# Kernel tuning notes

Measured on AMD Instinct MI355X. Metric: run time of the kernel, lower is better.

The kernel has to match this reference:

```python
import jax, jax.numpy as jnp
import numpy as np

B, S = 2048, 512
VOCAB, MAXPOS = 50000, 512
DE = 50          # each embedding dim; concat -> 100
DIN, H, OUT = 100, 512, 2


def setup_inputs() -> dict:
    key = jax.random.key(0)
    ks = jax.random.split(key, 12)
    inp = {
        "emb_table": jax.random.normal(ks[0], (VOCAB, DE), jnp.float32) * 0.02,
        "pos_table": jax.random.normal(ks[1], (MAXPOS, DE), jnp.float32) * 0.02,
        "W1": jax.random.normal(ks[2], (DIN, H), jnp.float32) / np.sqrt(DIN),
        "b1": jnp.zeros((H,), jnp.float32),
        "W2": jax.random.normal(ks[3], (H, H), jnp.float32) / np.sqrt(H),
        "b2": jnp.zeros((H,), jnp.float32),
        "W3": jax.random.normal(ks[4], (H, H), jnp.float32) / np.sqrt(H),
        "b3": jnp.zeros((H,), jnp.float32),
        "Wf": jax.random.normal(ks[5], (H, OUT), jnp.float32) / np.sqrt(H),
        "bf": jnp.zeros((OUT,), jnp.float32),
        "seq": jax.random.randint(ks[6], (B, S), 0, VOCAB),
        "seq_length": jax.random.randint(ks[7], (B,), 1, S + 1),  # >=1 to avoid div-by-zero, as in real data
        "pos": jnp.tile(jnp.arange(S, dtype=jnp.int64 if jax.config.jax_enable_x64 else jnp.int32)[None, :], (B, 1)),
    }
    return inp


def reference(emb_table, pos_table, W1, b1, W2, b2, W3, b3, Wf, bf,
              seq, seq_length, pos):
    # Embedding lookups + concat on feature dim -> [B, S, 100]
    x = jnp.concatenate([emb_table[seq], pos_table[pos]], axis=2)
    # Masked mean over the first seq_length[i] tokens (replaces the Python double loop)
    mask = (jnp.arange(S)[None, :] < seq_length[:, None]).astype(x.dtype)  # [B, S]
    pooled = jnp.einsum("bsd,bs->bd", x, mask) / seq_length[:, None].astype(x.dtype)  # [B, 100]
    # MLP stack (Dropout p=0.5 is identity in eval mode)
    h = jax.nn.relu(pooled @ W1 + b1)
    h = jax.nn.relu(h @ W2 + b2)
    h = jax.nn.relu(h @ W3 + b3)
    return h @ Wf + bf  # [B, OUT]
```

## Files before the change

### kernel.cpp

```cpp
#include <hip/hip_runtime.h>

typedef __attribute__((ext_vector_type(8))) short bf16x8;
typedef __attribute__((ext_vector_type(4))) float f32x4;

#define B_    2048
#define S_    512

#define OFF_WF1   0u
#define OFF_WF2   131072u
#define OFF_WF3   655360u
#define OFF_WFF   1179648u
#define OFF_PREF  1196032u
#define OFF_EMBB  1327104u
#define WS_NEED   (OFF_EMBB + 6400000u)

__device__ __forceinline__ unsigned short f2bf(float f) {
    unsigned int u = __float_as_uint(f);
    u += 0x7FFFu + ((u >> 16) & 1u);
    return (unsigned short)(u >> 16);
}

#define MFMA16(a, b, c) __builtin_amdgcn_mfma_f32_16x16x32_bf16((a), (b), (c), 0, 0, 0)

__global__ __launch_bounds__(256) void prep_convert(
    const float* __restrict__ W1, const float* __restrict__ W2,
    const float* __restrict__ W3, const float* __restrict__ Wf,
    const float* __restrict__ post, const int* __restrict__ pos,
    const float* __restrict__ emb,
    unsigned short* __restrict__ ws, float* __restrict__ pref, int do_emb)
{
    const int bid = blockIdx.x;
    const int tid = threadIdx.x;

    if (bid < 152) {
        __shared__ float tile[64][65];
        const float* src; unsigned short* dst;
        int k0, n0, Ksrc, Nsrc, ksTot, nTiles;
        if (bid < 64)       { src=W2; dst=ws+OFF_WF2/2; k0=(bid>>3)*64; n0=(bid&7)*64; Ksrc=512; Nsrc=512; ksTot=16; nTiles=4; }
        else if (bid < 128) { int b=bid-64;  src=W3; dst=ws+OFF_WF3/2; k0=(b>>3)*64; n0=(b&7)*64; Ksrc=512; Nsrc=512; ksTot=16; nTiles=4; }
        else if (bid < 144) { int b=bid-128; src=W1; dst=ws+OFF_WF1/2; k0=(b>>3)*64; n0=(b&7)*64; Ksrc=100; Nsrc=512; ksTot=4;  nTiles=4; }
        else                { int b=bid-144; src=Wf; dst=ws+OFF_WFF/2; k0=b*64;      n0=0;        Ksrc=512; Nsrc=2;   ksTot=16; nTiles=1; }

        const int c  = tid & 63;
        const int r4 = tid >> 6;
#pragma unroll
        for (int rr = 0; rr < 16; ++rr) {
            int r = rr*4 + r4;
            float v = 0.f;
            if (k0 + r < Ksrc && n0 + c < Nsrc) v = src[(size_t)(k0+r)*Nsrc + n0 + c];
            tile[r][c] = v;
        }
        __syncthreads();
        const int nWords = nTiles * 2 * 64;
        for (int w = tid; w < nWords; w += 256) {
            int lane = w & 63, ks_l = (w >> 6) & 1, nt_l = w >> 7;
            int kr = ks_l*32 + ((lane >> 4) << 3);
            int nc = nt_l*16 + (lane & 15);
            uint4 wv;
            wv.x = (unsigned)f2bf(tile[kr+0][nc]) | ((unsigned)f2bf(tile[kr+1][nc]) << 16);
            wv.y = (unsigned)f2bf(tile[kr+2][nc]) | ((unsigned)f2bf(tile[kr+3][nc]) << 16);
            wv.z = (unsigned)f2bf(tile[kr+4][nc]) | ((unsigned)f2bf(tile[kr+5][nc]) << 16);
            wv.w = (unsigned)f2bf(tile[kr+6][nc]) | ((unsigned)f2bf(tile[kr+7][nc]) << 16);
            int ntile = (n0 >> 4) + nt_l, ks = (k0 >> 5) + ks_l;
            ((uint4*)dst)[(size_t)(ntile*ksTot + ks)*64 + lane] = wv;
        }
    } else if (bid == 152) {
        __shared__ int   idx_s[512];
        __shared__ float csum[4][52];
        idx_s[tid]       = pos[tid];
        idx_s[tid + 256] = pos[tid + 256];
        __syncthreads();
        const int c = tid >> 6, d = tid & 63;
        if (d < 50) {
            float run = 0.f;
            for (int s = c*128; s < c*128 + 128; ++s)
                run += post[(size_t)idx_s[s]*50 + d];
            csum[c][d] = run;
        }
        __syncthreads();
        if (d < 50) {
            float run = 0.f;
            for (int cc = 0; cc < c; ++cc) run += csum[cc][d];
            for (int s = c*128; s < c*128 + 128; ++s) {
                run += post[(size_t)idx_s[s]*50 + d];
                pref[(size_t)s*64 + d] = run;
            }
        }
    } else {
        if (!do_emb) return;
        unsigned short* embb = ws + OFF_EMBB/2;
        const int blk = bid - 153;
        const int r0  = blk * 128;
        if (r0 >= 50000) return;
        const int nr = min(128, 50000 - r0);
        for (int i = tid; i < nr * 64; i += 256) {
            int r = i >> 6, d = i & 63;
            float v = (d < 50) ? emb[(size_t)(r0 + r)*50 + d] : 0.f;
            embb[(size_t)(r0 + r)*64 + d] = f2bf(v);
        }
    }
}

__device__ __forceinline__ void load_afrags(bf16x8 (&a)[16],
    const unsigned short* h, int row, int kq)
{
#pragma unroll
    for (int ks = 0; ks < 16; ++ks)
        a[ks] = *(const bf16x8*)((const char*)h +
                  (((unsigned)(row * 1024 + ks * 64 + kq * 16)) ^ ((row & 7) << 4)));
}

__device__ __forceinline__ void store_h(unsigned short* h, const f32x4 (&acc)[4],
    const float (&bb)[4], int wave, int row, int kq)
{
#pragma unroll
    for (int nt = 0; nt < 4; ++nt) {
        int c = wave*64 + nt*16 + row;
#pragma unroll
        for (int r4 = 0; r4 < 4; ++r4) {
            int hrow = kq*4 + r4;
            unsigned base = hrow * 1024;
            *(unsigned short*)((char*)h + ((base + c*2) ^ ((hrow & 7) << 4))) =
                f2bf(fmaxf(acc[nt][r4] + bb[nt], 0.f));
        }
    }
}

__device__ __forceinline__ void layer512(
    const bf16x8 (&a)[16], const unsigned short* __restrict__ Wfrag,
    const float* __restrict__ bias, unsigned short* hout,
    int wave, int row, int kq, int lane)
{
    const bf16x8* bp = (const bf16x8*)Wfrag + ((size_t)(wave*4) * 16 * 64) + lane;
    float bb[4];
#pragma unroll
    for (int nt = 0; nt < 4; ++nt) bb[nt] = bias[wave*64 + nt*16 + row];

    bf16x8 bvA[16], bvB[16];
#pragma unroll
    for (int ks = 0; ks < 16; ++ks) bvA[ks] = bp[(0*16 + ks)*64];
#pragma unroll
    for (int ks = 0; ks < 16; ++ks) bvB[ks] = bp[(1*16 + ks)*64];

    f32x4 acc[4];
    acc[0] = (f32x4){0.f,0.f,0.f,0.f};
#pragma unroll
    for (int ks = 0; ks < 16; ++ks) acc[0] = MFMA16(a[ks], bvA[ks], acc[0]);
#pragma unroll
    for (int ks = 0; ks < 16; ++ks) bvA[ks] = bp[(2*16 + ks)*64];

    acc[1] = (f32x4){0.f,0.f,0.f,0.f};
#pragma unroll
    for (int ks = 0; ks < 16; ++ks) acc[1] = MFMA16(a[ks], bvB[ks], acc[1]);
#pragma unroll
    for (int ks = 0; ks < 16; ++ks) bvB[ks] = bp[(3*16 + ks)*64];

    acc[2] = (f32x4){0.f,0.f,0.f,0.f};
#pragma unroll
    for (int ks = 0; ks < 16; ++ks) acc[2] = MFMA16(a[ks], bvA[ks], acc[2]);
    acc[3] = (f32x4){0.f,0.f,0.f,0.f};
#pragma unroll
    for (int ks = 0; ks < 16; ++ks) acc[3] = MFMA16(a[ks], bvB[ks], acc[3]);

    store_h(hout, acc, bb, wave, row, kq);
}

template<int EMODE>
__global__ __launch_bounds__(512, 2) void dan_fused(
    const float* __restrict__ emb, const int* __restrict__ seq,
    const int* __restrict__ seqlen, const unsigned short* __restrict__ ws_ro,
    const float* __restrict__ pref,
    const float* __restrict__ b1, const float* __restrict__ b2,
    const float* __restrict__ b3, const float* __restrict__ bfin,
    float* __restrict__ out)
{
    __shared__ __align__(16) unsigned short idx_s[8*512];
    __shared__ __align__(16) unsigned short pooled_s[16*144];
    __shared__ __align__(16) unsigned short hA[8192];
    __shared__ __align__(16) unsigned short hB[8192];

    const int tid  = threadIdx.x;
    const int wave = tid >> 6;
    const int lane = tid & 63;
    const int row  = lane & 15;
    const int kq   = lane >> 4;
    const int b0   = blockIdx.x * 8;

    const unsigned short* WF1 = ws_ro + OFF_WF1 / 2;
    const unsigned short* WF2 = ws_ro + OFF_WF2 / 2;
    const unsigned short* WF3 = ws_ro + OFF_WF3 / 2;
    const unsigned short* WFF = ws_ro + OFF_WFF / 2;

    for (int i = tid; i < 8*512; i += 512)
        idx_s[i] = (unsigned short)seq[(size_t)b0 * S_ + i];
    for (int i = tid; i < 16*144; i += 512) pooled_s[i] = 0;

    bf16x8 w1f[4][4];
    {
        const bf16x8* bp1 = (const bf16x8*)WF1 + ((size_t)(wave*4) * 4 * 64) + lane;
#pragma unroll
        for (int ci = 0; ci < 4; ++ci)
#pragma unroll
            for (int ks = 0; ks < 4; ++ks) w1f[ci][ks] = bp1[(ci*4 + ks)*64];
    }
    __syncthreads();

    const int L = seqlen[b0 + wave];
    const float Lf = (float)L;
    const unsigned short* idxr = idx_s + wave * 512;

    if (EMODE == 0) {
        const int tg = lane >> 3, dq = lane & 7;
        const uint4* tbl = (const uint4*)(ws_ro + OFF_EMBB / 2);
        float acc8[8];
#pragma unroll
        for (int j = 0; j < 8; ++j) acc8[j] = 0.f;

        const int Lfull = L & ~63;
        for (int s0 = 0; s0 < Lfull; s0 += 64) {
            uint4 q[8];
#pragma unroll
            for (int u = 0; u < 8; ++u) {
                int tok = idxr[s0 + u*8 + tg];
                q[u] = tbl[(size_t)tok * 8 + dq];
            }
#pragma unroll
            for (int u = 0; u < 8; ++u) {
                unsigned dw[4] = {q[u].x, q[u].y, q[u].z, q[u].w};
#pragma unroll
                for (int v = 0; v < 4; ++v) {
                    acc8[2*v]   += __uint_as_float(dw[v] << 16);
                    acc8[2*v+1] += __uint_as_float(dw[v] & 0xffff0000u);
                }
            }
        }
        for (int s0 = Lfull; s0 < L; s0 += 8) {
            int s = s0 + tg;
            uint4 q = {0u,0u,0u,0u};
            if (s < L) q = tbl[(size_t)idxr[s] * 8 + dq];
            unsigned dw[4] = {q.x, q.y, q.z, q.w};
#pragma unroll
            for (int v = 0; v < 4; ++v) {
                acc8[2*v]   += __uint_as_float(dw[v] << 16);
                acc8[2*v+1] += __uint_as_float(dw[v] & 0xffff0000u);
            }
        }
#pragma unroll
        for (int j = 0; j < 8; ++j) acc8[j] += __shfl_xor(acc8[j], 8);
#pragma unroll
        for (int j = 0; j < 8; ++j) acc8[j] += __shfl_xor(acc8[j], 16);
#pragma unroll
        for (int j = 0; j < 8; ++j) acc8[j] += __shfl_xor(acc8[j], 32);
        if (lane < 8) {
#pragma unroll
            for (int j = 0; j < 8; ++j) {
                int d = lane*8 + j;
                if (d < 50) pooled_s[wave*144 + d] = f2bf(acc8[j] / Lf);
            }
        }
    } else {
        float accE = 0.f;
        for (int s = 0; s < L; ++s) {
            int tok = idxr[s];
            if (lane < 50) accE += emb[(size_t)tok*50 + lane];
        }
        if (lane < 50) pooled_s[wave*144 + lane] = f2bf(accE / Lf);
    }
    if (lane < 50)
        pooled_s[wave*144 + 50 + lane] = f2bf(pref[(size_t)(L-1)*64 + lane] / Lf);
    __syncthreads();

    {
        bf16x8 a1[4];
#pragma unroll
        for (int ks = 0; ks < 4; ++ks)
            a1[ks] = *(const bf16x8*)&pooled_s[row*144 + ks*32 + kq*8];
        f32x4 acc[4];
        float bb[4];
#pragma unroll
        for (int ci = 0; ci < 4; ++ci) {
            bb[ci] = b1[wave*64 + ci*16 + row];
            acc[ci] = (f32x4){0.f,0.f,0.f,0.f};
#pragma unroll
            for (int ks = 0; ks < 4; ++ks) acc[ci] = MFMA16(a1[ks], w1f[ci][ks], acc[ci]);
        }
        store_h(hA, acc, bb, wave, row, kq);
    }
    __syncthreads();

    bf16x8 a[16];
    load_afrags(a, hA, row, kq);
    layer512(a, WF2, b2, hB, wave, row, kq, lane);
    __syncthreads();

    load_afrags(a, hB, row, kq);
    layer512(a, WF3, b3, hA, wave, row, kq, lane);
    __syncthreads();

    if (wave == 0) {
        load_afrags(a, hA, row, kq);
        const bf16x8* bpf = (const bf16x8*)WFF + lane;
        f32x4 accf = {0.f, 0.f, 0.f, 0.f};
#pragma unroll
        for (int ks = 0; ks < 16; ++ks) {
            bf16x8 bv = bpf[ks*64];
            accf = MFMA16(a[ks], bv, accf);
        }
        if (row < 2 && kq < 2) {
            float bb = bfin[row];
#pragma unroll
            for (int r4 = 0; r4 < 4; ++r4) {
                int m = kq*4 + r4;
                out[(size_t)(b0 + m) * 2 + row] = accf[r4] + bb;
            }
        }
    }
}

extern "C" void kernel_launch(void* const* d_in, const int* in_sizes, int n_in,
                              void* d_out, int out_size, void* d_ws, size_t ws_size,
                              hipStream_t stream)
{
    const float* emb    = (const float*)d_in[0];
    const float* post   = (const float*)d_in[1];
    const float* W1     = (const float*)d_in[2];
    const float* b1     = (const float*)d_in[3];
    const float* W2     = (const float*)d_in[4];
    const float* b2     = (const float*)d_in[5];
    const float* W3     = (const float*)d_in[6];
    const float* b3     = (const float*)d_in[7];
    const float* Wf     = (const float*)d_in[8];
    const float* bf     = (const float*)d_in[9];
    const int*   seq    = (const int*)d_in[10];
    const int*   seqlen = (const int*)d_in[11];
    const int*   pos    = (const int*)d_in[12];
    float*       out    = (float*)d_out;

    unsigned short* ws = (unsigned short*)d_ws;
    float* pref = (float*)((char*)d_ws + OFF_PREF);
    const int do_emb = (ws_size >= (size_t)WS_NEED) ? 1 : 0;

    prep_convert<<<544, 256, 0, stream>>>(W1, W2, W3, Wf, post, pos, emb,
                                          ws, pref, do_emb);
    if (do_emb)
        dan_fused<0><<<B_ / 8, 512, 0, stream>>>(emb, seq, seqlen, ws, pref,
                                                 b1, b2, b3, bf, out);
    else
        dan_fused<1><<<B_ / 8, 512, 0, stream>>>(emb, seq, seqlen, ws, pref,
                                                 b1, b2, b3, bf, out);
}
```

Measured before the change: 47.76 us.

## Split fused MLP into pooling kernel plus per-layer tiled GEMM kernels

Breaks the single fused kernel, where each 8-row block streamed full 512x512 weight matrices from global memory, into a pool+layer1 kernel and two layer kernels. Each layer kernel stages a 64-column weight slice into LDS with global_load_lds and reuses it across 64 batch rows. Hidden activations go through workspace in MFMA fragment layout. The final 512x2 projection is folded into the layer-3 epilogue with shuffles and atomicAdd into an output pre-seeded with the bias. The cost is two extra launches, global round trips for the activations, and nondeterministic float atomics.

```diff
diff --git a/kernel.cpp b/kernel.cpp
--- a/kernel.cpp
+++ b/kernel.cpp
@@ -9,9 +9,10 @@
 #define OFF_WF1   0u
 #define OFF_WF2   131072u
 #define OFF_WF3   655360u
-#define OFF_WFF   1179648u
-#define OFF_PREF  1196032u
-#define OFF_EMBB  1327104u
+#define OFF_PREF  1179648u
+#define OFF_H1F   1310720u
+#define OFF_H2F   3407872u
+#define OFF_EMBB  5505024u
 #define WS_NEED   (OFF_EMBB + 6400000u)
 
 __device__ __forceinline__ unsigned short f2bf(float f) {
@@ -24,7 +25,7 @@
 
 __global__ __launch_bounds__(256) void prep_convert(
     const float* __restrict__ W1, const float* __restrict__ W2,
-    const float* __restrict__ W3, const float* __restrict__ Wf,
+    const float* __restrict__ W3,
     const float* __restrict__ post, const int* __restrict__ pos,
     const float* __restrict__ emb,
     unsigned short* __restrict__ ws, float* __restrict__ pref, int do_emb)
@@ -32,14 +33,13 @@
     const int bid = blockIdx.x;
     const int tid = threadIdx.x;
 
-    if (bid < 152) {
+    if (bid < 144) {
         __shared__ float tile[64][65];
         const float* src; unsigned short* dst;
-        int k0, n0, Ksrc, Nsrc, ksTot, nTiles;
-        if (bid < 64)       { src=W2; dst=ws+OFF_WF2/2; k0=(bid>>3)*64; n0=(bid&7)*64; Ksrc=512; Nsrc=512; ksTot=16; nTiles=4; }
-        else if (bid < 128) { int b=bid-64;  src=W3; dst=ws+OFF_WF3/2; k0=(b>>3)*64; n0=(b&7)*64; Ksrc=512; Nsrc=512; ksTot=16; nTiles=4; }
-        else if (bid < 144) { int b=bid-128; src=W1; dst=ws+OFF_WF1/2; k0=(b>>3)*64; n0=(b&7)*64; Ksrc=100; Nsrc=512; ksTot=4;  nTiles=4; }
-        else                { int b=bid-144; src=Wf; dst=ws+OFF_WFF/2; k0=b*64;      n0=0;        Ksrc=512; Nsrc=2;   ksTot=16; nTiles=1; }
+        int k0, n0, Ksrc, ksTot;
+        if (bid < 64)       { src=W2; dst=ws+OFF_WF2/2; k0=(bid>>3)*64; n0=(bid&7)*64; Ksrc=512; ksTot=16; }
+        else if (bid < 128) { int b=bid-64;  src=W3; dst=ws+OFF_WF3/2; k0=(b>>3)*64; n0=(b&7)*64; Ksrc=512; ksTot=16; }
+        else                { int b=bid-128; src=W1; dst=ws+OFF_WF1/2; k0=(b>>3)*64; n0=(b&7)*64; Ksrc=100; ksTot=4;  }
 
         const int c  = tid & 63;
         const int r4 = tid >> 6;
@@ -47,12 +47,11 @@
         for (int rr = 0; rr < 16; ++rr) {
             int r = rr*4 + r4;
             float v = 0.f;
-            if (k0 + r < Ksrc && n0 + c < Nsrc) v = src[(size_t)(k0+r)*Nsrc + n0 + c];
+            if (k0 + r < Ksrc) v = src[(size_t)(k0+r)*512 + n0 + c];
             tile[r][c] = v;
         }
         __syncthreads();
-        const int nWords = nTiles * 2 * 64;
-        for (int w = tid; w < nWords; w += 256) {
+        for (int w = tid; w < 8*64; w += 256) {
             int lane = w & 63, ks_l = (w >> 6) & 1, nt_l = w >> 7;
             int kr = ks_l*32 + ((lane >> 4) << 3);
             int nc = nt_l*16 + (lane & 15);
@@ -64,7 +63,7 @@
             int ntile = (n0 >> 4) + nt_l, ks = (k0 >> 5) + ks_l;
             ((uint4*)dst)[(size_t)(ntile*ksTot + ks)*64 + lane] = wv;
         }
-    } else if (bid == 152) {
+    } else if (bid == 144) {
         __shared__ int   idx_s[512];
         __shared__ float csum[4][52];
         idx_s[tid]       = pos[tid];
@@ -89,7 +88,7 @@
     } else {
         if (!do_emb) return;
         unsigned short* embb = ws + OFF_EMBB/2;
-        const int blk = bid - 153;
+        const int blk = bid - 145;
         const int r0  = blk * 128;
         if (r0 >= 50000) return;
         const int nr = min(128, 50000 - r0);
@@ -101,99 +100,32 @@
     }
 }
 
-__device__ __forceinline__ void load_afrags(bf16x8 (&a)[16],
-    const unsigned short* h, int row, int kq)
-{
-#pragma unroll
-    for (int ks = 0; ks < 16; ++ks)
-        a[ks] = *(const bf16x8*)((const char*)h +
-                  (((unsigned)(row * 1024 + ks * 64 + kq * 16)) ^ ((row & 7) << 4)));
-}
-
-__device__ __forceinline__ void store_h(unsigned short* h, const f32x4 (&acc)[4],
-    const float (&bb)[4], int wave, int row, int kq)
-{
-#pragma unroll
-    for (int nt = 0; nt < 4; ++nt) {
-        int c = wave*64 + nt*16 + row;
-#pragma unroll
-        for (int r4 = 0; r4 < 4; ++r4) {
-            int hrow = kq*4 + r4;
-            unsigned base = hrow * 1024;
-            *(unsigned short*)((char*)h + ((base + c*2) ^ ((hrow & 7) << 4))) =
-                f2bf(fmaxf(acc[nt][r4] + bb[nt], 0.f));
-        }
-    }
-}
-
-__device__ __forceinline__ void layer512(
-    const bf16x8 (&a)[16], const unsigned short* __restrict__ Wfrag,
-    const float* __restrict__ bias, unsigned short* hout,
-    int wave, int row, int kq, int lane)
-{
-    const bf16x8* bp = (const bf16x8*)Wfrag + ((size_t)(wave*4) * 16 * 64) + lane;
-    float bb[4];
-#pragma unroll
-    for (int nt = 0; nt < 4; ++nt) bb[nt] = bias[wave*64 + nt*16 + row];
-
-    bf16x8 bvA[16], bvB[16];
-#pragma unroll
-    for (int ks = 0; ks < 16; ++ks) bvA[ks] = bp[(0*16 + ks)*64];
-#pragma unroll
-    for (int ks = 0; ks < 16; ++ks) bvB[ks] = bp[(1*16 + ks)*64];
-
-    f32x4 acc[4];
-    acc[0] = (f32x4){0.f,0.f,0.f,0.f};
-#pragma unroll
-    for (int ks = 0; ks < 16; ++ks) acc[0] = MFMA16(a[ks], bvA[ks], acc[0]);
-#pragma unroll
-    for (int ks = 0; ks < 16; ++ks) bvA[ks] = bp[(2*16 + ks)*64];
-
-    acc[1] = (f32x4){0.f,0.f,0.f,0.f};
-#pragma unroll
-    for (int ks = 0; ks < 16; ++ks) acc[1] = MFMA16(a[ks], bvB[ks], acc[1]);
-#pragma unroll
-    for (int ks = 0; ks < 16; ++ks) bvB[ks] = bp[(3*16 + ks)*64];
-
-    acc[2] = (f32x4){0.f,0.f,0.f,0.f};
-#pragma unroll
-    for (int ks = 0; ks < 16; ++ks) acc[2] = MFMA16(a[ks], bvA[ks], acc[2]);
-    acc[3] = (f32x4){0.f,0.f,0.f,0.f};
-#pragma unroll
-    for (int ks = 0; ks < 16; ++ks) acc[3] = MFMA16(a[ks], bvB[ks], acc[3]);
-
-    store_h(hout, acc, bb, wave, row, kq);
-}
-
 template<int EMODE>
-__global__ __launch_bounds__(512, 2) void dan_fused(
+__global__ __launch_bounds__(512, 2) void pool_l1(
     const float* __restrict__ emb, const int* __restrict__ seq,
     const int* __restrict__ seqlen, const unsigned short* __restrict__ ws_ro,
-    const float* __restrict__ pref,
-    const float* __restrict__ b1, const float* __restrict__ b2,
-    const float* __restrict__ b3, const float* __restrict__ bfin,
+    unsigned short* __restrict__ ws_rw, const float* __restrict__ pref,
+    const float* __restrict__ b1, const float* __restrict__ bfin,
     float* __restrict__ out)
 {
     __shared__ __align__(16) unsigned short idx_s[8*512];
     __shared__ __align__(16) unsigned short pooled_s[16*144];
-    __shared__ __align__(16) unsigned short hA[8192];
-    __shared__ __align__(16) unsigned short hB[8192];
+    __shared__ __align__(16) char tbuf[8*2304];
 
     const int tid  = threadIdx.x;
     const int wave = tid >> 6;
     const int lane = tid & 63;
     const int row  = lane & 15;
     const int kq   = lane >> 4;
-    const int b0   = blockIdx.x * 8;
+    const int blk  = blockIdx.x;
+    const int b0   = blk * 8;
 
     const unsigned short* WF1 = ws_ro + OFF_WF1 / 2;
-    const unsigned short* WF2 = ws_ro + OFF_WF2 / 2;
-    const unsigned short* WF3 = ws_ro + OFF_WF3 / 2;
-    const unsigned short* WFF = ws_ro + OFF_WFF / 2;
 
     for (int i = tid; i < 8*512; i += 512)
         idx_s[i] = (unsigned short)seq[(size_t)b0 * S_ + i];
     for (int i = tid; i < 16*144; i += 512) pooled_s[i] = 0;
+    if (tid < 16) out[b0*2 + tid] = bfin[tid & 1];
 
     bf16x8 w1f[4][4];
     {
@@ -270,48 +202,129 @@
         pooled_s[wave*144 + 50 + lane] = f2bf(pref[(size_t)(L-1)*64 + lane] / Lf);
     __syncthreads();
 
+    bf16x8 a1[4];
+#pragma unroll
+    for (int ks = 0; ks < 4; ++ks)
+        a1[ks] = *(const bf16x8*)&pooled_s[row*144 + ks*32 + kq*8];
+
+    char* tb = tbuf + wave*2304;
+#pragma unroll
+    for (int ci = 0; ci < 4; ++ci) {
+        const float bb = b1[wave*64 + ci*16 + row];
+        f32x4 acc = (f32x4){0.f,0.f,0.f,0.f};
+#pragma unroll
+        for (int ks = 0; ks < 4; ++ks) acc = MFMA16(a1[ks], w1f[ci][ks], acc);
+#pragma unroll
+        for (int r = 0; r < 4; ++r)
+            *(unsigned short*)(tb + (kq*4 + r)*144 + (ci*16 + row)*2) =
+                f2bf(fmaxf(acc[r] + bb, 0.f));
+    }
+
+    unsigned short* h1f = ws_rw + OFF_H1F/2;
+    const int bt = blk >> 1;
+    const bool mine = ((row >> 3) == (blk & 1));
+    const int lr = row & 7;
+#pragma unroll
+    for (int ksl = 0; ksl < 2; ++ksl) {
+        bf16x8 wv = *(const bf16x8*)(tb + lr*144 + ksl*64 + kq*16);
+        if (mine)
+            ((bf16x8*)h1f)[(size_t)(bt*16 + wave*2 + ksl)*64 + lane] = wv;
+    }
+}
+
+template<int LAYER>
+__global__ __launch_bounds__(512, 2) void layer_kernel(
+    const unsigned short* __restrict__ ws_ro, unsigned short* __restrict__ ws_rw,
+    const float* __restrict__ bias, const float* __restrict__ Wf,
+    float* __restrict__ out)
+{
+    __shared__ __align__(16) char Bst[65536];
+    __shared__ __align__(16) char tbuf[8*1536];
+
+    const int tid  = threadIdx.x;
+    const int wave = tid >> 6;
+    const int lane = tid & 63;
+    const int row  = lane & 15;
+    const int kq   = lane >> 4;
+    const int mb   = blockIdx.x >> 3;
+    const int nb   = blockIdx.x & 7;
+    const int mw   = wave >> 1;
+    const int nw   = wave & 1;
+    const int bt   = mb*4 + mw;
+
+    const unsigned short* WF = ws_ro + (LAYER==2 ? OFF_WF2 : OFF_WF3)/2;
+    const bf16x8* hin = (const bf16x8*)(ws_ro + (LAYER==2 ? OFF_H1F : OFF_H2F)/2);
+
     {
-        bf16x8 a1[4];
-#pragma unroll
-        for (int ks = 0; ks < 4; ++ks)
-            a1[ks] = *(const bf16x8*)&pooled_s[row*144 + ks*32 + kq*8];
-        f32x4 acc[4];
-        float bb[4];
-#pragma unroll
-        for (int ci = 0; ci < 4; ++ci) {
-            bb[ci] = b1[wave*64 + ci*16 + row];
-            acc[ci] = (f32x4){0.f,0.f,0.f,0.f};
-#pragma unroll
-            for (int ks = 0; ks < 4; ++ks) acc[ci] = MFMA16(a1[ks], w1f[ci][ks], acc[ci]);
-        }
-        store_h(hA, acc, bb, wave, row, kq);
-    }
+        const char* src = (const char*)WF + (size_t)(nb*4) * 16 * 1024;
+#pragma unroll
+        for (int it = 0; it < 8; ++it)
+            __builtin_amdgcn_global_load_lds(
+                (const __attribute__((address_space(1))) unsigned int*)(src + it*8192 + tid*16),
+                (__attribute__((address_space(3))) unsigned int*)(Bst + it*8192 + tid*16),
+                16, 0, 0);
+    }
+
+    bf16x8 a[16];
+#pragma unroll
+    for (int ks = 0; ks < 16; ++ks)
+        a[ks] = hin[(size_t)(bt*16 + ks)*64 + lane];
     __syncthreads();
 
-    bf16x8 a[16];
-    load_afrags(a, hA, row, kq);
-    layer512(a, WF2, b2, hB, wave, row, kq, lane);
-    __syncthreads();
-
-    load_afrags(a, hB, row, kq);
-    layer512(a, WF3, b3, hA, wave, row, kq, lane);
-    __syncthreads();
-
-    if (wave == 0) {
-        load_afrags(a, hA, row, kq);
-        const bf16x8* bpf = (const bf16x8*)WFF + lane;
-        f32x4 accf = {0.f, 0.f, 0.f, 0.f};
-#pragma unroll
-        for (int ks = 0; ks < 16; ++ks) {
-            bf16x8 bv = bpf[ks*64];
-            accf = MFMA16(a[ks], bv, accf);
-        }
-        if (row < 2 && kq < 2) {
-            float bb = bfin[row];
-#pragma unroll
-            for (int r4 = 0; r4 < 4; ++r4) {
-                int m = kq*4 + r4;
-                out[(size_t)(b0 + m) * 2 + row] = accf[r4] + bb;
+    f32x4 acc0 = (f32x4){0.f,0.f,0.f,0.f};
+    f32x4 acc1 = (f32x4){0.f,0.f,0.f,0.f};
+    const char* bp0 = Bst + (size_t)(nw*2 + 0)*16*1024 + lane*16;
+    const char* bp1 = Bst + (size_t)(nw*2 + 1)*16*1024 + lane*16;
+#pragma unroll
+    for (int ks = 0; ks < 16; ++ks) {
+        bf16x8 bv0 = *(const bf16x8*)(bp0 + ks*1024);
+        bf16x8 bv1 = *(const bf16x8*)(bp1 + ks*1024);
+        acc0 = MFMA16(a[ks], bv0, acc0);
+        acc1 = MFMA16(a[ks], bv1, acc1);
+    }
+
+    const int nt0 = nb*4 + nw*2, nt1 = nt0 + 1;
+    const float bb0 = bias[nt0*16 + row], bb1 = bias[nt1*16 + row];
+
+    if (LAYER == 2) {
+        char* tb = tbuf + wave*1536;
+#pragma unroll
+        for (int r = 0; r < 4; ++r) {
+            *(unsigned short*)(tb + (kq*4 + r)*96 + row*2) =
+                f2bf(fmaxf(acc0[r] + bb0, 0.f));
+            *(unsigned short*)(tb + (kq*4 + r)*96 + (16 + row)*2) =
+                f2bf(fmaxf(acc1[r] + bb1, 0.f));
+        }
+        bf16x8 wv = *(const bf16x8*)(tb + row*96 + kq*16);
+        unsigned short* h2f = ws_rw + OFF_H2F/2;
+        ((bf16x8*)h2f)[(size_t)(bt*16 + nb*2 + nw)*64 + lane] = wv;
+    } else {
+        float v0[4], v1[4];
+#pragma unroll
+        for (int r = 0; r < 4; ++r) {
+            v0[r] = fmaxf(acc0[r] + bb0, 0.f);
+            v1[r] = fmaxf(acc1[r] + bb1, 0.f);
+        }
+        const float2 wf0 = ((const float2*)Wf)[nt0*16 + row];
+        const float2 wf1 = ((const float2*)Wf)[nt1*16 + row];
+        float po[4][2];
+#pragma unroll
+        for (int r = 0; r < 4; ++r) {
+            po[r][0] = v0[r]*wf0.x + v1[r]*wf1.x;
+            po[r][1] = v0[r]*wf0.y + v1[r]*wf1.y;
+        }
+#pragma unroll
+        for (int s = 1; s < 16; s <<= 1)
+#pragma unroll
+            for (int r = 0; r < 4; ++r) {
+                po[r][0] += __shfl_xor(po[r][0], s);
+                po[r][1] += __shfl_xor(po[r][1], s);
+            }
+        if (row == 0) {
+#pragma unroll
+            for (int r = 0; r < 4; ++r) {
+                atomicAdd(&out[(size_t)(bt*16 + kq*4 + r)*2 + 0], po[r][0]);
+                atomicAdd(&out[(size_t)(bt*16 + kq*4 + r)*2 + 1], po[r][1]);
             }
         }
     }
@@ -340,12 +353,14 @@
     float* pref = (float*)((char*)d_ws + OFF_PREF);
     const int do_emb = (ws_size >= (size_t)WS_NEED) ? 1 : 0;
 
-    prep_convert<<<544, 256, 0, stream>>>(W1, W2, W3, Wf, post, pos, emb,
+    prep_convert<<<536, 256, 0, stream>>>(W1, W2, W3, post, pos, emb,
                                           ws, pref, do_emb);
     if (do_emb)
-        dan_fused<0><<<B_ / 8, 512, 0, stream>>>(emb, seq, seqlen, ws, pref,
-                                                 b1, b2, b3, bf, out);
+        pool_l1<0><<<256, 512, 0, stream>>>(emb, seq, seqlen, ws, ws, pref,
+                                            b1, bf, out);
     else
-        dan_fused<1><<<B_ / 8, 512, 0, stream>>>(emb, seq, seqlen, ws, pref,
-                                                 b1, b2, b3, bf, out);
-}
+        pool_l1<1><<<256, 512, 0, stream>>>(emb, seq, seqlen, ws, ws, pref,
+                                            b1, bf, out);
+    layer_kernel<2><<<256, 512, 0, stream>>>(ws, ws, b2, Wf, out);
+    layer_kernel<3><<<256, 512, 0, stream>>>(ws, ws, b3, Wf, out);
+}
```

Result: slower. 53.46 us (+11.9%).
